# Performance work log

Hardware: AMD Instinct MI355X
Metric: run time of the kernel (lower is better)

## Reference

```python
import jax, jax.numpy as jnp
import numpy as np

N, E, D_IN, L, H, U = 20000, 320000, 256, 4, 4, 64
HID = H * U  # 256
OUT = 64
LN_EPS = 1e-3  # keras LayerNormalization default epsilon
NEG_SLOPE = 0.2


def layer_norm(x, g, b):
    m = jnp.mean(x, axis=-1, keepdims=True)
    v = jnp.var(x, axis=-1, keepdims=True)
    return (x - m) * jax.lax.rsqrt(v + LN_EPS) * g + b


def gatv2(x, dst, src, Wl, Wr, a):
    # x: [N, HID]; Wl/Wr: [HID, H, U]; a: [H, U]
    zl = jnp.einsum('nd,dhu->nhu', x, Wl)  # target projection
    zr = jnp.einsum('nd,dhu->nhu', x, Wr)  # source projection / messages
    f = jax.nn.leaky_relu(zl[dst] + zr[src], NEG_SLOPE)       # [E, H, U]
    s = jnp.einsum('ehu,hu->eh', f, a)                        # [E, H]
    smax = jax.ops.segment_max(s, dst, num_segments=N)        # [N, H]
    es = jnp.exp(s - smax[dst])
    denom = jax.ops.segment_sum(es, dst, num_segments=N)      # [N, H]
    agg = jax.ops.segment_sum(es[:, :, None] * zr[src], dst, num_segments=N)
    agg = agg / (denom[:, :, None] + 1e-9)                    # [N, H, U]
    return agg.reshape(N, HID) + x  # residual (input dim == H*U)


def setup_inputs() -> dict:
    key = jax.random.key(0)
    ks = jax.random.split(key, 10)
    s_in = 1.0 / np.sqrt(D_IN)
    s_h = 1.0 / np.sqrt(HID)
    return {
        'x': jax.random.normal(ks[0], (N, D_IN), jnp.float32),
        'head_W': jax.random.normal(ks[1], (D_IN, HID), jnp.float32) * s_in,
        'head_b': jnp.zeros((HID,), jnp.float32),
        'ng_g': jnp.ones((L, HID), jnp.float32),
        'ng_b': jnp.zeros((L, HID), jnp.float32),
        'Wl': jax.random.normal(ks[2], (L, HID, H, U), jnp.float32) * s_h,
        'Wr': jax.random.normal(ks[3], (L, HID, H, U), jnp.float32) * s_h,
        'att': jax.random.normal(ks[4], (L, H, U), jnp.float32) * (1.0 / np.sqrt(U)),
        'nd_g': jnp.ones((L, HID), jnp.float32),
        'nd_b': jnp.zeros((L, HID), jnp.float32),
        'dense_W': jax.random.normal(ks[5], (L, HID, 4 * HID), jnp.float32) * s_h,
        'dense_b': jnp.zeros((L, 4 * HID), jnp.float32),
        'tail_W': jax.random.normal(ks[6], (HID, OUT), jnp.float32) * s_h,
        'tail_b': jnp.zeros((OUT,), jnp.float32),
        'edges': jax.random.randint(ks[7], (E, 2), 0, N, jnp.int32),
    }


def reference(x, head_W, head_b, ng_g, ng_b, Wl, Wr, att, nd_g, nd_b,
              dense_W, dense_b, tail_W, tail_b, edges):
    dst, src = edges[:, 0], edges[:, 1]
    h = x @ head_W + head_b  # head_layer
    for l in range(L):
        h = layer_norm(h, ng_g[l], ng_b[l])
        h = gatv2(h, dst, src, Wl[l], Wr[l], att[l])
        xr = layer_norm(h, nd_g[l], nd_b[l])
        # inference: dropout is identity
        d = jax.nn.gelu(xr @ dense_W[l] + dense_b[l], approximate=True)  # [N, 4*HID]
        h = d.reshape(N, 4, HID).sum(axis=1) + xr  # Add(split(.,4)) + residual
    return h @ tail_W + tail_b
```

## Files before the change

### kernel.cpp

```cpp
#include <hip/hip_runtime.h>
#include <cstdint>

#define NN 20000
#define EE 320000
#define DHID 256

typedef short bf16x8 __attribute__((ext_vector_type(8)));
typedef float f32x4 __attribute__((ext_vector_type(4)));


__device__ __forceinline__ float b2f(unsigned short u) {
    union { unsigned int i; float f; } v;
    v.i = ((unsigned int)u) << 16;
    return v.f;
}

__device__ __forceinline__ void b2f2(unsigned int w, float& lo, float& hi) {
    union { unsigned int i; float f; } a, c;
    a.i = w << 16;
    c.i = w & 0xffff0000u;
    lo = a.f;
    hi = c.f;
}

__device__ __forceinline__ unsigned short f2b(float x) {
    union { float f; unsigned int i; } v;
    v.f = x;
    unsigned int r = (v.i + 0x7FFFu + ((v.i >> 16) & 1u)) >> 16;
    return (unsigned short)r;
}

__device__ __forceinline__ float wave_sum(float v) {
#pragma unroll
    for (int m = 1; m < 64; m <<= 1) v += __shfl_xor(v, m);
    return v;
}

__device__ __forceinline__ float quad16_sum(float v) {
#pragma unroll
    for (int m = 1; m < 16; m <<= 1) v += __shfl_xor(v, m);
    return v;
}

__device__ __forceinline__ float gelu_f(float x) {
    float z = 0.7978845608028654f * (x + 0.044715f * x * x * x);
    float e = __expf(2.0f * z);
    float t = 1.0f - 2.0f / (e + 1.0f);
    return 0.5f * x * (1.0f + t);
}

__device__ __forceinline__ void gld16(const unsigned short* g, unsigned short* lds) {
    __builtin_amdgcn_global_load_lds((const __attribute__((address_space(1))) unsigned int*)g,
                                     (__attribute__((address_space(3))) unsigned int*)lds, 16, 0, 0);
}


__global__ void hist_kernel(const int* __restrict__ edges, int* __restrict__ counts, int E_) {
    int e = blockIdx.x * 256 + threadIdx.x;
    if (e >= E_) return;
    atomicAdd(&counts[edges[e * 2]], 1);
}

__global__ void pad_counts(const int* __restrict__ counts, int* __restrict__ pc, int n) {
    int i = blockIdx.x * 256 + threadIdx.x;
    if (i < n) pc[i] = (counts[i] + 3) & ~3;
}

__global__ __launch_bounds__(1024) void scan_block(const int* __restrict__ counts,
                                                   int* __restrict__ excl,
                                                   int* __restrict__ bsums, int n) {
    __shared__ int sd[1024];
    int tid = threadIdx.x;
    int i = blockIdx.x * 1024 + tid;
    int c = (i < n) ? counts[i] : 0;
    sd[tid] = c;
    __syncthreads();
#pragma unroll
    for (int off = 1; off < 1024; off <<= 1) {
        int v = (tid >= off) ? sd[tid - off] : 0;
        __syncthreads();
        sd[tid] += v;
        __syncthreads();
    }
    if (i < n) excl[i] = sd[tid] - c;
    if (tid == 1023) bsums[blockIdx.x] = sd[1023];
}

__global__ void scan_tops(int* __restrict__ bsums, int nb) {
    if (threadIdx.x == 0 && blockIdx.x == 0) {
        int run = 0;
        for (int i = 0; i < nb; ++i) { int t = bsums[i]; bsums[i] = run; run += t; }
    }
}

__global__ void scan_fix2(const int* __restrict__ excl, const int* __restrict__ bsums,
                          const int* __restrict__ counts,
                          int* __restrict__ astart, int* __restrict__ aend,
                          int* __restrict__ cursor, int n) {
    int i = blockIdx.x * 256 + threadIdx.x;
    if (i < n) {
        int v = excl[i] + bsums[i >> 10];
        astart[i] = v;
        cursor[i] = v;
        aend[i]   = v + counts[i];
    }
}

__global__ void scatter2(const int* __restrict__ edges, int* __restrict__ cursor,
                         unsigned int* __restrict__ soff, int E_) {
    int e = blockIdx.x * 256 + threadIdx.x;
    if (e >= E_) return;
    int dstn = edges[e * 2];
    int src  = edges[e * 2 + 1];
    int pos = atomicAdd(&cursor[dstn], 1);
    soff[pos] = (unsigned int)src << 10;
}


__global__ __launch_bounds__(256) void transpose_bf16(const float* __restrict__ W,
                                                      unsigned short* __restrict__ Wt,
                                                      int K, int M, size_t lsW, size_t lsT) {
    W  += (size_t)blockIdx.z * lsW;
    Wt += (size_t)blockIdx.z * lsT;
    __shared__ float sm[32][33];
    int m0 = blockIdx.x * 32, k0 = blockIdx.y * 32;
    int tx = threadIdx.x & 31, ty = threadIdx.x >> 5;
#pragma unroll
    for (int i = 0; i < 4; ++i)
        sm[ty + i * 8][tx] = W[(size_t)(k0 + ty + i * 8) * M + m0 + tx];
    __syncthreads();
#pragma unroll
    for (int i = 0; i < 4; ++i)
        Wt[(size_t)(m0 + ty + i * 8) * K + k0 + tx] = f2b(sm[tx][ty + i * 8]);
}

__global__ __launch_bounds__(256) void transpose_perm(const float* __restrict__ W,
                                                      unsigned short* __restrict__ Wt,
                                                      int K, int M, size_t lsW, size_t lsT) {
    W  += (size_t)blockIdx.z * lsW;
    Wt += (size_t)blockIdx.z * lsT;
    __shared__ float sm[32][33];
    int m0 = blockIdx.x * 32, k0 = blockIdx.y * 32;
    int tx = threadIdx.x & 31, ty = threadIdx.x >> 5;
#pragma unroll
    for (int i = 0; i < 4; ++i)
        sm[ty + i * 8][tx] = W[(size_t)(k0 + ty + i * 8) * M + m0 + tx];
    __syncthreads();
#pragma unroll
    for (int i = 0; i < 4; ++i) {
        int mm = m0 + ty + i * 8;
        int c = mm >> 8, j = mm & 255;
        int by = j >> 5, t = j & 31;
        int cc = (by << 7) | ((t >> 4) << 6) | (c << 4) | (t & 15);
        Wt[(size_t)cc * K + k0 + tx] = f2b(sm[tx][ty + i * 8]);
    }
}

__global__ void convert_bf16(const float* __restrict__ in, unsigned short* __restrict__ out, int n4) {
    int i = blockIdx.x * 256 + threadIdx.x;
    if (i >= n4) return;
    float4 v = *(const float4*)(in + (size_t)i * 4);
    ushort4 o;
    o.x = f2b(v.x); o.y = f2b(v.y); o.z = f2b(v.z); o.w = f2b(v.w);
    *(ushort4*)(out + (size_t)i * 4) = o;
}


__global__ __launch_bounds__(256) void ln_kernel(const float* __restrict__ X,
                                                 const float* __restrict__ g,
                                                 const float* __restrict__ b,
                                                 unsigned short* __restrict__ Yb, int nrows) {
    int row = blockIdx.x * 4 + (threadIdx.x >> 6);
    int lane = threadIdx.x & 63;
    if (row >= nrows) return;
    float4 v = *(const float4*)(X + (size_t)row * DHID + lane * 4);
    float sum = wave_sum(v.x + v.y + v.z + v.w);
    float sq  = wave_sum(v.x * v.x + v.y * v.y + v.z * v.z + v.w * v.w);
    float mean = sum * (1.0f / DHID);
    float var  = sq * (1.0f / DHID) - mean * mean;
    float r = rsqrtf(fmaxf(var, 0.0f) + 1e-3f);
    float4 gv = *(const float4*)(g + lane * 4);
    float4 bv = *(const float4*)(b + lane * 4);
    float4 o;
    o.x = (v.x - mean) * r * gv.x + bv.x;
    o.y = (v.y - mean) * r * gv.y + bv.y;
    o.z = (v.z - mean) * r * gv.z + bv.z;
    o.w = (v.w - mean) * r * gv.w + bv.w;
    ushort4 ob;
    ob.x = f2b(o.x); ob.y = f2b(o.y); ob.z = f2b(o.z); ob.w = f2b(o.w);
    *(ushort4*)(Yb + (size_t)row * DHID + lane * 4) = ob;
}

__global__ __launch_bounds__(256) void ln_dense(const unsigned short* __restrict__ d,
                                                const unsigned short* __restrict__ xrb,
                                                const float* __restrict__ g,
                                                const float* __restrict__ b,
                                                unsigned short* __restrict__ Yb, int nrows) {
    int row = blockIdx.x * 4 + (threadIdx.x >> 6);
    int lane = threadIdx.x & 63;
    if (row >= nrows) return;
    ushort4 xu = *(const ushort4*)(xrb + (size_t)row * DHID + lane * 4);
    ushort4 du = *(const ushort4*)(d   + (size_t)row * DHID + lane * 4);
    float4 v;
    v.x = b2f(xu.x) + b2f(du.x);
    v.y = b2f(xu.y) + b2f(du.y);
    v.z = b2f(xu.z) + b2f(du.z);
    v.w = b2f(xu.w) + b2f(du.w);
    float sum = wave_sum(v.x + v.y + v.z + v.w);
    float sq  = wave_sum(v.x * v.x + v.y * v.y + v.z * v.z + v.w * v.w);
    float mean = sum * (1.0f / DHID);
    float var  = sq * (1.0f / DHID) - mean * mean;
    float r = rsqrtf(fmaxf(var, 0.0f) + 1e-3f);
    float4 gv = *(const float4*)(g + lane * 4);
    float4 bv = *(const float4*)(b + lane * 4);
    float4 o;
    o.x = (v.x - mean) * r * gv.x + bv.x;
    o.y = (v.y - mean) * r * gv.y + bv.y;
    o.z = (v.z - mean) * r * gv.z + bv.z;
    o.w = (v.w - mean) * r * gv.w + bv.w;
    ushort4 ob;
    ob.x = f2b(o.x); ob.y = f2b(o.y); ob.z = f2b(o.z); ob.w = f2b(o.w);
    *(ushort4*)(Yb + (size_t)row * DHID + lane * 4) = ob;
}

__global__ __launch_bounds__(256) void combine_final(const unsigned short* __restrict__ d,
                                                     const unsigned short* __restrict__ xrb,
                                                     unsigned short* __restrict__ hb, int nrows) {
    int row = blockIdx.x * 4 + (threadIdx.x >> 6);
    int lane = threadIdx.x & 63;
    if (row >= nrows) return;
    ushort4 xu = *(const ushort4*)(xrb + (size_t)row * DHID + lane * 4);
    ushort4 du = *(const ushort4*)(d   + (size_t)row * DHID + lane * 4);
    ushort4 ob;
    ob.x = f2b(b2f(xu.x) + b2f(du.x));
    ob.y = f2b(b2f(xu.y) + b2f(du.y));
    ob.z = f2b(b2f(xu.z) + b2f(du.z));
    ob.w = f2b(b2f(xu.w) + b2f(du.w));
    *(ushort4*)(hb + (size_t)row * DHID + lane * 4) = ob;
}


#define CS_STRIDE 140
#define CS2_STRIDE 40

template <int EP>
__global__ __launch_bounds__(256, 3) void gemm128(const unsigned short* __restrict__ A,
                                                  const unsigned short* __restrict__ B,
                                                  const float* __restrict__ bias,
                                                  void* __restrict__ Cv, int nrows, int ncols) {
    __shared__ unsigned short smem[128 * CS_STRIDE];
    unsigned short* As = smem;
    unsigned short* Bs = smem + 8192;
    unsigned short* Cs = smem;
    const int bm = blockIdx.x * 128, bn = blockIdx.y * 128;
    if (bm >= nrows) return;
    const int tid  = threadIdx.x;
    const int w    = tid >> 6, lane = tid & 63;
    const int quad = lane >> 4, l16 = lane & 15;
    const int wm = w >> 1, wn = w & 1;

    const int srow = lane & 15;
    const int sg   = lane >> 4;
    int ga0 = min(bm + w * 32 + srow,      nrows - 1);
    int ga1 = min(bm + w * 32 + 16 + srow, nrows - 1);
    int gb0 = min(bn + w * 32 + srow,      ncols - 1);
    int gb1 = min(bn + w * 32 + 16 + srow, ncols - 1);
    const unsigned short* Ap0 = A + (size_t)ga0 * 256 + sg * 8;
    const unsigned short* Ap1 = A + (size_t)ga1 * 256 + sg * 8;
    const unsigned short* Bp0 = B + (size_t)gb0 * 256 + sg * 8;
    const unsigned short* Bp1 = B + (size_t)gb1 * 256 + sg * 8;
    unsigned short* la0 = As + (2 * w) * 1024;
    unsigned short* la1 = As + (2 * w + 1) * 1024;
    unsigned short* lb0 = Bs + (2 * w) * 1024;
    unsigned short* lb1 = Bs + (2 * w + 1) * 1024;

    f32x4 acc[4][4] = {};
    for (int k0 = 0; k0 < 256; k0 += 64) {
        gld16(Ap0 + k0,      la0);
        gld16(Ap0 + k0 + 32, la0 + 512);
        gld16(Ap1 + k0,      la1);
        gld16(Ap1 + k0 + 32, la1 + 512);
        gld16(Bp0 + k0,      lb0);
        gld16(Bp0 + k0 + 32, lb0 + 512);
        gld16(Bp1 + k0,      lb1);
        gld16(Bp1 + k0 + 32, lb1 + 512);
        __syncthreads();
#pragma unroll
        for (int kk = 0; kk < 2; ++kk) {
            bf16x8 a[4], b[4];
#pragma unroll
            for (int mi = 0; mi < 4; ++mi)
                a[mi] = *(const bf16x8*)(As + (wm * 4 + mi) * 1024 + (kk * 4 + quad) * 128 + l16 * 8);
#pragma unroll
            for (int ni = 0; ni < 4; ++ni)
                b[ni] = *(const bf16x8*)(Bs + (wn * 4 + ni) * 1024 + (kk * 4 + quad) * 128 + l16 * 8);
#pragma unroll
            for (int mi = 0; mi < 4; ++mi)
#pragma unroll
                for (int ni = 0; ni < 4; ++ni)
                    acc[mi][ni] = __builtin_amdgcn_mfma_f32_16x16x32_bf16(a[mi], b[ni], acc[mi][ni], 0, 0, 0);
        }
        __syncthreads();
    }

    if (EP == 0) {
#pragma unroll
        for (int ni = 0; ni < 4; ++ni) {
            int col = bn + wn * 64 + ni * 16 + l16;
            if (col >= ncols) continue;
            float bv = bias ? bias[col] : 0.0f;
#pragma unroll
            for (int mi = 0; mi < 4; ++mi) {
#pragma unroll
                for (int r = 0; r < 4; ++r) {
                    int row = bm + wm * 64 + mi * 16 + quad * 4 + r;
                    if (row < nrows) ((float*)Cv)[(size_t)row * ncols + col] = acc[mi][ni][r] + bv;
                }
            }
        }
    } else if (EP == 1) {
#pragma unroll
        for (int ni = 0; ni < 4; ++ni) {
            int lc = wn * 64 + ni * 16 + l16;
#pragma unroll
            for (int mi = 0; mi < 4; ++mi) {
#pragma unroll
                for (int r = 0; r < 4; ++r) {
                    int lr = wm * 64 + mi * 16 + quad * 4 + r;
                    Cs[lr * CS_STRIDE + lc] = f2b(acc[mi][ni][r]);
                }
            }
        }
        __syncthreads();
#pragma unroll
        for (int i = 0; i < 8; ++i) {
            int id = tid + 256 * i;
            int lr = id >> 4;
            int lc = (id & 15) * 8;
            int grow = bm + lr;
            if (grow < nrows) {
                uint4 val = *(const uint4*)(Cs + lr * CS_STRIDE + lc);
                *(uint4*)((unsigned short*)Cv + (size_t)grow * ncols + bn + lc) = val;
            }
        }
    } else {
        unsigned short* Cs2 = smem;
        int jfl = wn * 16 + l16;
        int jf  = (bn >> 2) + jfl;
        float bv0 = bias[jf];
        float bv1 = bias[256 + jf];
        float bv2 = bias[512 + jf];
        float bv3 = bias[768 + jf];
#pragma unroll
        for (int mi = 0; mi < 4; ++mi) {
#pragma unroll
            for (int r = 0; r < 4; ++r) {
                float v = gelu_f(acc[mi][0][r] + bv0) + gelu_f(acc[mi][1][r] + bv1)
                        + gelu_f(acc[mi][2][r] + bv2) + gelu_f(acc[mi][3][r] + bv3);
                int lr = wm * 64 + mi * 16 + quad * 4 + r;
                Cs2[lr * CS2_STRIDE + jfl] = f2b(v);
            }
        }
        __syncthreads();
#pragma unroll
        for (int i = 0; i < 2; ++i) {
            int id = tid + 256 * i;
            int lr = id >> 2;
            int q  = id & 3;
            int grow = bm + lr;
            if (grow < nrows) {
                uint4 val = *(const uint4*)(Cs2 + lr * CS2_STRIDE + q * 8);
                *(uint4*)((unsigned short*)Cv + (size_t)grow * 256 + (bn >> 2) + q * 8) = val;
            }
        }
    }
}


__global__ __launch_bounds__(256) void gat_fused(const unsigned short* __restrict__ zb,
                                                 const float* __restrict__ att,
                                                 const unsigned int* __restrict__ soff,
                                                 const int* __restrict__ astart,
                                                 const int* __restrict__ aend,
                                                 const unsigned short* __restrict__ hnb,
                                                 const float* __restrict__ g,
                                                 const float* __restrict__ b,
                                                 unsigned short* __restrict__ xrb, int nrows) {
    int wid = threadIdx.x >> 6;
    int lane = threadIdx.x & 63;
    int n = blockIdx.x * 4 + wid;
    if (n >= nrows) return;
    int p0  = astart[n];
    int end = aend[n];

    ushort4 zlu = *(const ushort4*)(zb + (size_t)n * 512 + lane * 4);
    float zl0 = b2f(zlu.x), zl1 = b2f(zlu.y), zl2 = b2f(zlu.z), zl3 = b2f(zlu.w);
    float4 a4 = *(const float4*)(att + lane * 4);

    const char* zrb = (const char*)zb + 512;
    const unsigned int loff = (unsigned int)lane * 8u;

    float denom = 0.f;
    float ax = 0.f, ay = 0.f, az = 0.f, aw = 0.f;

    auto edge4 = [&](uint2 u0, uint2 u1, uint2 u2, uint2 u3, int pb) {
        float z00, z01, z02, z03, z10, z11, z12, z13;
        float z20, z21, z22, z23, z30, z31, z32, z33;
        b2f2(u0.x, z00, z01); b2f2(u0.y, z02, z03);
        b2f2(u1.x, z10, z11); b2f2(u1.y, z12, z13);
        b2f2(u2.x, z20, z21); b2f2(u2.y, z22, z23);
        b2f2(u3.x, z30, z31); b2f2(u3.y, z32, z33);

        float v00 = zl0 + z00, v01 = zl1 + z01, v02 = zl2 + z02, v03 = zl3 + z03;
        float v10 = zl0 + z10, v11 = zl1 + z11, v12 = zl2 + z12, v13 = zl3 + z13;
        float v20 = zl0 + z20, v21 = zl1 + z21, v22 = zl2 + z22, v23 = zl3 + z23;
        float v30 = zl0 + z30, v31 = zl1 + z31, v32 = zl2 + z32, v33 = zl3 + z33;
        v00 = fmaxf(v00, 0.2f * v00); v01 = fmaxf(v01, 0.2f * v01);
        v02 = fmaxf(v02, 0.2f * v02); v03 = fmaxf(v03, 0.2f * v03);
        v10 = fmaxf(v10, 0.2f * v10); v11 = fmaxf(v11, 0.2f * v11);
        v12 = fmaxf(v12, 0.2f * v12); v13 = fmaxf(v13, 0.2f * v13);
        v20 = fmaxf(v20, 0.2f * v20); v21 = fmaxf(v21, 0.2f * v21);
        v22 = fmaxf(v22, 0.2f * v22); v23 = fmaxf(v23, 0.2f * v23);
        v30 = fmaxf(v30, 0.2f * v30); v31 = fmaxf(v31, 0.2f * v31);
        v32 = fmaxf(v32, 0.2f * v32); v33 = fmaxf(v33, 0.2f * v33);
        float q0 = a4.x * v00 + a4.y * v01 + a4.z * v02 + a4.w * v03;
        float q1 = a4.x * v10 + a4.y * v11 + a4.z * v12 + a4.w * v13;
        float q2 = a4.x * v20 + a4.y * v21 + a4.z * v22 + a4.w * v23;
        float q3 = a4.x * v30 + a4.y * v31 + a4.z * v32 + a4.w * v33;
        float s0 = quad16_sum(q0);
        float s1 = quad16_sum(q1);
        float s2 = quad16_sum(q2);
        float s3 = quad16_sum(q3);
        float w0 = __expf(s0);
        float w1 = (pb + 1 < end) ? __expf(s1) : 0.0f;
        float w2 = (pb + 2 < end) ? __expf(s2) : 0.0f;
        float w3 = (pb + 3 < end) ? __expf(s3) : 0.0f;
        denom += (w0 + w1) + (w2 + w3);
        ax += (w0 * z00 + w1 * z10) + (w2 * z20 + w3 * z30);
        ay += (w0 * z01 + w1 * z11) + (w2 * z21 + w3 * z31);
        az += (w0 * z02 + w1 * z12) + (w2 * z22 + w3 * z32);
        aw += (w0 * z03 + w1 * z13) + (w2 * z23 + w3 * z33);
    };

    uint4 oA = *(const uint4*)(soff + p0);
    uint2 cA0 = *(const uint2*)(zrb + (oA.x + loff));
    uint2 cA1 = *(const uint2*)(zrb + (oA.y + loff));
    uint2 cA2 = *(const uint2*)(zrb + (oA.z + loff));
    uint2 cA3 = *(const uint2*)(zrb + (oA.w + loff));
    uint4 oB = *(const uint4*)(soff + p0 + 4);
    uint2 cB0 = *(const uint2*)(zrb + (oB.x + loff));
    uint2 cB1 = *(const uint2*)(zrb + (oB.y + loff));
    uint2 cB2 = *(const uint2*)(zrb + (oB.z + loff));
    uint2 cB3 = *(const uint2*)(zrb + (oB.w + loff));

    for (int p = p0; p < end; p += 8) {
        edge4(cA0, cA1, cA2, cA3, p);
        oA = *(const uint4*)(soff + p + 8);
        cA0 = *(const uint2*)(zrb + (oA.x + loff));
        cA1 = *(const uint2*)(zrb + (oA.y + loff));
        cA2 = *(const uint2*)(zrb + (oA.z + loff));
        cA3 = *(const uint2*)(zrb + (oA.w + loff));
        if (p + 4 >= end) break;
        edge4(cB0, cB1, cB2, cB3, p + 4);
        oB = *(const uint4*)(soff + p + 12);
        cB0 = *(const uint2*)(zrb + (oB.x + loff));
        cB1 = *(const uint2*)(zrb + (oB.y + loff));
        cB2 = *(const uint2*)(zrb + (oB.z + loff));
        cB3 = *(const uint2*)(zrb + (oB.w + loff));
    }

    size_t idx = (size_t)n * DHID + lane * 4;
    ushort4 ru = *(const ushort4*)(hnb + idx);
    float inv = 1.0f / (denom + 1e-9f);
    float4 o;
    o.x = ax * inv + b2f(ru.x);
    o.y = ay * inv + b2f(ru.y);
    o.z = az * inv + b2f(ru.z);
    o.w = aw * inv + b2f(ru.w);
    float sum = wave_sum(o.x + o.y + o.z + o.w);
    float sq  = wave_sum(o.x * o.x + o.y * o.y + o.z * o.z + o.w * o.w);
    float mean = sum * (1.0f / DHID);
    float var  = sq * (1.0f / DHID) - mean * mean;
    float rnorm = rsqrtf(fmaxf(var, 0.0f) + 1e-3f);
    float4 gv = *(const float4*)(g + lane * 4);
    float4 bv = *(const float4*)(b + lane * 4);
    float4 y;
    y.x = (o.x - mean) * rnorm * gv.x + bv.x;
    y.y = (o.y - mean) * rnorm * gv.y + bv.y;
    y.z = (o.z - mean) * rnorm * gv.z + bv.z;
    y.w = (o.w - mean) * rnorm * gv.w + bv.w;
    ushort4 ob;
    ob.x = f2b(y.x); ob.y = f2b(y.y); ob.z = f2b(y.z); ob.w = f2b(y.w);
    *(ushort4*)(xrb + idx) = ob;
}


extern "C" void kernel_launch(void* const* d_in, const int* in_sizes, int n_in,
                              void* d_out, int out_size, void* d_ws, size_t ws_size,
                              hipStream_t stream) {
    const float* x       = (const float*)d_in[0];
    const float* head_W  = (const float*)d_in[1];
    const float* head_b  = (const float*)d_in[2];
    const float* ng_g    = (const float*)d_in[3];
    const float* ng_b    = (const float*)d_in[4];
    const float* Wl      = (const float*)d_in[5];
    const float* Wr      = (const float*)d_in[6];
    const float* att     = (const float*)d_in[7];
    const float* nd_g    = (const float*)d_in[8];
    const float* nd_b    = (const float*)d_in[9];
    const float* dense_W = (const float*)d_in[10];
    const float* dense_b = (const float*)d_in[11];
    const float* tail_W  = (const float*)d_in[12];
    const float* tail_b  = (const float*)d_in[13];
    const int*   edges   = (const int*)d_in[14];
    float* out = (float*)d_out;

    const size_t NH = (size_t)NN * DHID;
    const int SOFF_LEN = EE + 4 * NN + 16;
    float* xr = (float*)d_ws;
    float* hn = xr + NH;
    unsigned short* hnb = (unsigned short*)(hn + NH);
    unsigned short* xrb = hnb + NH;
    unsigned short* U   = xrb + NH;
    unsigned short* zb  = U;
    unsigned short* d_buf = U;
    unsigned short* headT  = U + 4 * NH;
    unsigned short* WzT    = headT + 65536;
    unsigned short* denseT = WzT + 524288;
    unsigned short* tailT  = denseT + 1048576;
    int* counts  = (int*)(tailT + 16384);
    int* pcounts = counts + NN;
    int* bsums   = pcounts + NN;
    int* excl    = bsums + 32;
    int* cursor  = excl + NN;
    unsigned int* soff = (unsigned int*)hn;
    int* astart = (int*)(soff + SOFF_LEN);
    int* aendp  = astart + NN;

    hipMemsetAsync(counts, 0, NN * sizeof(int), stream);
    hipMemsetAsync(soff, 0, SOFF_LEN * sizeof(int), stream);
    hist_kernel<<<(EE + 255) / 256, 256, 0, stream>>>(edges, counts, EE);
    pad_counts<<<(NN + 255) / 256, 256, 0, stream>>>(counts, pcounts, NN);
    scan_block<<<(NN + 1023) / 1024, 1024, 0, stream>>>(pcounts, excl, bsums, NN);
    scan_tops<<<1, 64, 0, stream>>>(bsums, (NN + 1023) / 1024);
    scan_fix2<<<(NN + 255) / 256, 256, 0, stream>>>(excl, bsums, counts, astart, aendp, cursor, NN);
    scatter2<<<(EE + 255) / 256, 256, 0, stream>>>(edges, cursor, soff, EE);

    transpose_bf16<<<dim3(8, 8, 1), 256, 0, stream>>>(head_W, headT, 256, 256, 0, 0);
    transpose_bf16<<<dim3(8, 8, 4), 256, 0, stream>>>(Wl, WzT, 256, 256, 65536, 131072);
    transpose_bf16<<<dim3(8, 8, 4), 256, 0, stream>>>(Wr, WzT + 65536, 256, 256, 65536, 131072);
    transpose_perm<<<dim3(32, 8, 4), 256, 0, stream>>>(dense_W, denseT, 256, 1024, 262144, 262144);
    transpose_bf16<<<dim3(2, 8, 1), 256, 0, stream>>>(tail_W, tailT, 256, 64, 0, 0);
    convert_bf16<<<(int)(NH / 4 + 255) / 256, 256, 0, stream>>>(x, hnb, (int)(NH / 4));

    const int GXP = 160;
    gemm128<0><<<dim3(GXP, 2), 256, 0, stream>>>(hnb, headT, head_b, xr, NN, 256);

    for (int l = 0; l < 4; ++l) {
        if (l == 0)
            ln_kernel<<<NN / 4, 256, 0, stream>>>(xr, ng_g, ng_b, hnb, NN);
        else
            ln_dense<<<NN / 4, 256, 0, stream>>>(d_buf, xrb, ng_g + l * 256, ng_b + l * 256, hnb, NN);
        gemm128<1><<<dim3(GXP, 4), 256, 0, stream>>>(hnb, WzT + (size_t)l * 131072, nullptr, zb, NN, 512);
        gat_fused<<<(NN + 3) / 4, 256, 0, stream>>>(zb, att + l * 256, soff, astart, aendp, hnb,
                                                    nd_g + l * 256, nd_b + l * 256, xrb, NN);
        gemm128<3><<<dim3(GXP, 8), 256, 0, stream>>>(xrb, denseT + (size_t)l * 262144,
                                                     dense_b + l * 1024, d_buf, NN, 1024);
    }
    combine_final<<<NN / 4, 256, 0, stream>>>(d_buf, xrb, hnb, NN);
    gemm128<0><<<dim3(GXP, 1), 256, 0, stream>>>(hnb, tailT, tail_b, out, NN, 64);
}
```

Before: 544.7 us.

## Widen GEMM tiles to 128x256 with 512-thread blocks and DPP quad reductions

Replaces the 128x128, 256-thread GEMM for the z-projection and dense layers with a 128x256 tile run by 512 threads. Each A tile is now loaded once per block and reused across twice as many output columns, which cuts the grid in half. The dense weight permutation is changed to match the wider tile, and the GELU-sum epilogue now writes 64-column chunks. Separately, the 16-lane reduction is switched from shfl_xor to DPP row_ror adds. The cost is more LDS and registers per block, plus a two-phase staged epilogue that adds extra barriers.

Result: slower. 570.6 us (+4.7%).

```diff
diff --git a/kernel.cpp b/kernel.cpp
--- a/kernel.cpp
+++ b/kernel.cpp
@@ -36,9 +36,14 @@
     return v;
 }
 
+#define DPP_ROR_ADD(v, n)                                                              \
+    v += __int_as_float(__builtin_amdgcn_update_dpp(__float_as_int(v), __float_as_int(v), \
+                                                    0x120 + (n), 0xF, 0xF, 0))
 __device__ __forceinline__ float quad16_sum(float v) {
-#pragma unroll
-    for (int m = 1; m < 16; m <<= 1) v += __shfl_xor(v, m);
+    DPP_ROR_ADD(v, 8);
+    DPP_ROR_ADD(v, 4);
+    DPP_ROR_ADD(v, 2);
+    DPP_ROR_ADD(v, 1);
     return v;
 }
 
@@ -150,8 +155,7 @@
     for (int i = 0; i < 4; ++i) {
         int mm = m0 + ty + i * 8;
         int c = mm >> 8, j = mm & 255;
-        int by = j >> 5, t = j & 31;
-        int cc = (by << 7) | ((t >> 4) << 6) | (c << 4) | (t & 15);
+        int cc = ((j >> 6) << 8) | (((j >> 4) & 3) << 6) | (c << 4) | (j & 15);
         Wt[(size_t)cc * K + k0 + tx] = f2b(sm[tx][ty + i * 8]);
     }
 }
@@ -241,17 +245,14 @@
 
 
 #define CS_STRIDE 140
-#define CS2_STRIDE 40
-
-template <int EP>
-__global__ __launch_bounds__(256, 3) void gemm128(const unsigned short* __restrict__ A,
-                                                  const unsigned short* __restrict__ B,
-                                                  const float* __restrict__ bias,
-                                                  void* __restrict__ Cv, int nrows, int ncols) {
+
+__global__ __launch_bounds__(256, 3) void gemm128f(const unsigned short* __restrict__ A,
+                                                   const unsigned short* __restrict__ B,
+                                                   const float* __restrict__ bias,
+                                                   float* __restrict__ C, int nrows, int ncols) {
     __shared__ unsigned short smem[128 * CS_STRIDE];
     unsigned short* As = smem;
     unsigned short* Bs = smem + 8192;
-    unsigned short* Cs = smem;
     const int bm = blockIdx.x * 128, bn = blockIdx.y * 128;
     if (bm >= nrows) return;
     const int tid  = threadIdx.x;
@@ -303,50 +304,116 @@
         __syncthreads();
     }
 
-    if (EP == 0) {
-#pragma unroll
-        for (int ni = 0; ni < 4; ++ni) {
-            int col = bn + wn * 64 + ni * 16 + l16;
-            if (col >= ncols) continue;
-            float bv = bias ? bias[col] : 0.0f;
-#pragma unroll
-            for (int mi = 0; mi < 4; ++mi) {
-#pragma unroll
-                for (int r = 0; r < 4; ++r) {
-                    int row = bm + wm * 64 + mi * 16 + quad * 4 + r;
-                    if (row < nrows) ((float*)Cv)[(size_t)row * ncols + col] = acc[mi][ni][r] + bv;
+#pragma unroll
+    for (int ni = 0; ni < 4; ++ni) {
+        int col = bn + wn * 64 + ni * 16 + l16;
+        if (col >= ncols) continue;
+        float bv = bias ? bias[col] : 0.0f;
+#pragma unroll
+        for (int mi = 0; mi < 4; ++mi) {
+#pragma unroll
+            for (int r = 0; r < 4; ++r) {
+                int row = bm + wm * 64 + mi * 16 + quad * 4 + r;
+                if (row < nrows) C[(size_t)row * ncols + col] = acc[mi][ni][r] + bv;
+            }
+        }
+    }
+}
+
+
+#define CSW_STRIDE 136
+#define CS3_STRIDE 72
+
+template <int EP>
+__global__ __launch_bounds__(512, 4) void gemmW(const unsigned short* __restrict__ A,
+                                                const unsigned short* __restrict__ B,
+                                                const float* __restrict__ bias,
+                                                unsigned short* __restrict__ C, int nrows, int ncols) {
+    __shared__ unsigned short smem[24576];
+    unsigned short* As = smem;
+    unsigned short* Bs = smem + 8192;
+    const int bm = blockIdx.x * 128, bn = blockIdx.y * 256;
+    if (bm >= nrows) return;
+    const int tid  = threadIdx.x;
+    const int w    = tid >> 6, lane = tid & 63;
+    const int quad = lane >> 4, l16 = lane & 15;
+    const int wm = w & 1, wn = w >> 1;
+
+    const int srow = lane & 15;
+    const int sg   = lane >> 4;
+    int ga  = min(bm + w * 16 + srow,      nrows - 1);
+    int gb0 = min(bn + w * 32 + srow,      ncols - 1);
+    int gb1 = min(bn + w * 32 + 16 + srow, ncols - 1);
+    const unsigned short* Ap  = A + (size_t)ga  * 256 + sg * 8;
+    const unsigned short* Bp0 = B + (size_t)gb0 * 256 + sg * 8;
+    const unsigned short* Bp1 = B + (size_t)gb1 * 256 + sg * 8;
+    unsigned short* la  = As + w * 1024;
+    unsigned short* lb0 = Bs + (2 * w) * 1024;
+    unsigned short* lb1 = Bs + (2 * w + 1) * 1024;
+
+    f32x4 acc[4][4] = {};
+    for (int k0 = 0; k0 < 256; k0 += 64) {
+        gld16(Ap + k0,       la);
+        gld16(Ap + k0 + 32,  la + 512);
+        gld16(Bp0 + k0,      lb0);
+        gld16(Bp0 + k0 + 32, lb0 + 512);
+        gld16(Bp1 + k0,      lb1);
+        gld16(Bp1 + k0 + 32, lb1 + 512);
+        __syncthreads();
+#pragma unroll
+        for (int kk = 0; kk < 2; ++kk) {
+            bf16x8 a[4], b[4];
+#pragma unroll
+            for (int mi = 0; mi < 4; ++mi)
+                a[mi] = *(const bf16x8*)(As + (wm * 4 + mi) * 1024 + (kk * 4 + quad) * 128 + l16 * 8);
+#pragma unroll
+            for (int ni = 0; ni < 4; ++ni)
+                b[ni] = *(const bf16x8*)(Bs + (wn * 4 + ni) * 1024 + (kk * 4 + quad) * 128 + l16 * 8);
+#pragma unroll
+            for (int mi = 0; mi < 4; ++mi)
+#pragma unroll
+                for (int ni = 0; ni < 4; ++ni)
+                    acc[mi][ni] = __builtin_amdgcn_mfma_f32_16x16x32_bf16(a[mi], b[ni], acc[mi][ni], 0, 0, 0);
+        }
+        __syncthreads();
+    }
+
+    if (EP == 1) {
+        unsigned short* Cs = smem;
+#pragma unroll
+        for (int g = 0; g < 2; ++g) {
+            if ((w >> 2) == g) {
+#pragma unroll
+                for (int ni = 0; ni < 4; ++ni) {
+                    int lc = (wn & 1) * 64 + ni * 16 + l16;
+#pragma unroll
+                    for (int mi = 0; mi < 4; ++mi) {
+#pragma unroll
+                        for (int r = 0; r < 4; ++r) {
+                            int lr = wm * 64 + mi * 16 + quad * 4 + r;
+                            Cs[lr * CSW_STRIDE + lc] = f2b(acc[mi][ni][r]);
+                        }
+                    }
                 }
             }
-        }
-    } else if (EP == 1) {
-#pragma unroll
-        for (int ni = 0; ni < 4; ++ni) {
-            int lc = wn * 64 + ni * 16 + l16;
-#pragma unroll
-            for (int mi = 0; mi < 4; ++mi) {
-#pragma unroll
-                for (int r = 0; r < 4; ++r) {
-                    int lr = wm * 64 + mi * 16 + quad * 4 + r;
-                    Cs[lr * CS_STRIDE + lc] = f2b(acc[mi][ni][r]);
+            __syncthreads();
+#pragma unroll
+            for (int i = 0; i < 4; ++i) {
+                int id = tid + 512 * i;
+                int lr = id >> 4;
+                int lc = (id & 15) * 8;
+                int grow = bm + lr;
+                if (grow < nrows) {
+                    uint4 val = *(const uint4*)(Cs + lr * CSW_STRIDE + lc);
+                    *(uint4*)(C + (size_t)grow * ncols + bn + g * 128 + lc) = val;
                 }
             }
-        }
-        __syncthreads();
-#pragma unroll
-        for (int i = 0; i < 8; ++i) {
-            int id = tid + 256 * i;
-            int lr = id >> 4;
-            int lc = (id & 15) * 8;
-            int grow = bm + lr;
-            if (grow < nrows) {
-                uint4 val = *(const uint4*)(Cs + lr * CS_STRIDE + lc);
-                *(uint4*)((unsigned short*)Cv + (size_t)grow * ncols + bn + lc) = val;
-            }
+            __syncthreads();
         }
     } else {
         unsigned short* Cs2 = smem;
-        int jfl = wn * 16 + l16;
-        int jf  = (bn >> 2) + jfl;
+        int fl = wn * 16 + l16;
+        int jf = (bn >> 2) + fl;
         float bv0 = bias[jf];
         float bv1 = bias[256 + jf];
         float bv2 = bias[512 + jf];
@@ -358,19 +425,19 @@
                 float v = gelu_f(acc[mi][0][r] + bv0) + gelu_f(acc[mi][1][r] + bv1)
                         + gelu_f(acc[mi][2][r] + bv2) + gelu_f(acc[mi][3][r] + bv3);
                 int lr = wm * 64 + mi * 16 + quad * 4 + r;
-                Cs2[lr * CS2_STRIDE + jfl] = f2b(v);
+                Cs2[lr * CS3_STRIDE + fl] = f2b(v);
             }
         }
         __syncthreads();
 #pragma unroll
         for (int i = 0; i < 2; ++i) {
-            int id = tid + 256 * i;
-            int lr = id >> 2;
-            int q  = id & 3;
+            int id = tid + 512 * i;
+            int lr = id >> 3;
+            int q  = id & 7;
             int grow = bm + lr;
             if (grow < nrows) {
-                uint4 val = *(const uint4*)(Cs2 + lr * CS2_STRIDE + q * 8);
-                *(uint4*)((unsigned short*)Cv + (size_t)grow * 256 + (bn >> 2) + q * 8) = val;
+                uint4 val = *(const uint4*)(Cs2 + lr * CS3_STRIDE + q * 8);
+                *(uint4*)(C + (size_t)grow * 256 + (bn >> 2) + q * 8) = val;
             }
         }
     }
@@ -554,19 +621,19 @@
     convert_bf16<<<(int)(NH / 4 + 255) / 256, 256, 0, stream>>>(x, hnb, (int)(NH / 4));
 
     const int GXP = 160;
-    gemm128<0><<<dim3(GXP, 2), 256, 0, stream>>>(hnb, headT, head_b, xr, NN, 256);
+    gemm128f<<<dim3(GXP, 2), 256, 0, stream>>>(hnb, headT, head_b, xr, NN, 256);
 
     for (int l = 0; l < 4; ++l) {
         if (l == 0)
             ln_kernel<<<NN / 4, 256, 0, stream>>>(xr, ng_g, ng_b, hnb, NN);
         else
             ln_dense<<<NN / 4, 256, 0, stream>>>(d_buf, xrb, ng_g + l * 256, ng_b + l * 256, hnb, NN);
-        gemm128<1><<<dim3(GXP, 4), 256, 0, stream>>>(hnb, WzT + (size_t)l * 131072, nullptr, zb, NN, 512);
+        gemmW<1><<<dim3(GXP, 2), 512, 0, stream>>>(hnb, WzT + (size_t)l * 131072, nullptr, zb, NN, 512);
         gat_fused<<<(NN + 3) / 4, 256, 0, stream>>>(zb, att + l * 256, soff, astart, aendp, hnb,
                                                     nd_g + l * 256, nd_b + l * 256, xrb, NN);
-        gemm128<3><<<dim3(GXP, 8), 256, 0, stream>>>(xrb, denseT + (size_t)l * 262144,
-                                                     dense_b + l * 1024, d_buf, NN, 1024);
+        gemmW<3><<<dim3(GXP, 4), 512, 0, stream>>>(xrb, denseT + (size_t)l * 262144,
+                                                   dense_b + l * 1024, d_buf, NN, 1024);
     }
     combine_final<<<NN / 4, 256, 0, stream>>>(d_buf, xrb, hnb, NN);
-    gemm128<0><<<dim3(GXP, 1), 256, 0, stream>>>(hnb, tailT, tail_b, out, NN, 64);
-}
+    gemm128f<<<dim3(GXP, 1), 256, 0, stream>>>(hnb, tailT, tail_b, out, NN, 64);
+}
```
